# Kernel tuning notes

Measured on AMD Instinct MI355X. Metric: run time of the kernel, lower is better.

The kernel has to match this reference:

```python
import jax, jax.numpy as jnp
import numpy as np

B = 128          # graphs
N = 512          # nodes per graph
NT = B * N       # total nodes = 65536
E = NT * 16      # total edges = 1048576
IN = 64
H = 128
OUT = 2
L = 4            # num_layers
RATIO = 0.8


def setup_inputs() -> dict:
    key = jax.random.key(0)
    ks = jax.random.split(key, 20)

    def w(k, shape, fan_in):
        return jax.random.normal(k, shape, jnp.float32) / np.sqrt(fan_in)

    x = jax.random.normal(ks[0], (NT, IN), jnp.float32)
    edge_index = jax.random.randint(ks[1], (2, E), 0, NT, dtype=jnp.int32)
    batch = (jnp.arange(NT) // N).astype(jnp.int32)  # equal-size graphs

    return {
        "x": x,
        "edge_index": edge_index,
        "batch": batch,
        # conv1: GraphConv(IN, H, aggr='mean') -> lin_rel (w/ bias) + lin_root (no bias)
        "W1_rel": w(ks[2], (IN, H), IN),
        "W1_root": w(ks[3], (IN, H), IN),
        "b1": jnp.zeros((H,), jnp.float32),
        # convs[0..2]: GraphConv(H, H, aggr='mean'), stacked
        "Wc_rel": w(ks[4], (L - 1, H, H), H),
        "Wc_root": w(ks[5], (L - 1, H, H), H),
        "bc": jnp.zeros((L - 1, H), jnp.float32),
        # SAGPooling score GNN: GraphConv(H, 1) with default aggr='add'
        "pw_rel": w(ks[6], (H,), H),
        "pw_root": w(ks[7], (H,), H),
        "pb": jnp.zeros((1,), jnp.float32),
        # MLP head
        "lin1_W": w(ks[8], (L * H, H), L * H),
        "lin1_b": jnp.zeros((H,), jnp.float32),
        "lin2_W": w(ks[9], (H, OUT), H),
        "lin2_b": jnp.zeros((OUT,), jnp.float32),
    }


def _graph_conv_mean(x, src, dst, emask, W_rel, W_root, b, n):
    # PyG GraphConv: lin_rel(mean_{j->i} x_j) + lin_root(x_i); masked edges excluded.
    msg = x[src] * emask[:, None]                                  # [E, D] gather
    s = jax.ops.segment_sum(msg, dst, num_segments=n)              # [n, D] scatter-add
    cnt = jax.ops.segment_sum(emask, dst, num_segments=n)          # [n]
    agg = s / jnp.maximum(cnt, 1.0)[:, None]                       # zero for isolated nodes
    return agg @ W_rel + x @ W_root + b


def reference(x, edge_index, batch, W1_rel, W1_root, b1, Wc_rel, Wc_root, bc,
              pw_rel, pw_root, pb, lin1_W, lin1_b, lin2_W, lin2_b):
    src = edge_index[0]
    dst = edge_index[1]
    emask = jnp.ones((E,), jnp.float32)
    n = NT
    npg = N  # nodes per graph (all graphs equal size)

    h = jax.nn.relu(_graph_conv_mean(x, src, dst, emask, W1_rel, W1_root, b1, n))
    xs = [h.reshape(B, npg, H).mean(axis=1)]  # global_mean_pool

    for i in range(L - 1):
        h = jax.nn.relu(_graph_conv_mean(h, src, dst, emask, Wc_rel[i], Wc_root[i], bc[i], n))
        xs.append(h.reshape(B, npg, H).mean(axis=1))
        if i % 2 == 0 and i < L - 2:
            # ---- SAGPooling: score via GraphConv(H,1) with add aggregation ----
            smsg = jax.ops.segment_sum(h[src] * emask[:, None], dst, num_segments=n)
            score = smsg @ pw_rel + h @ pw_root + pb[0]            # [n]
            k = int(np.ceil(RATIO * npg))
            topv, topi = jax.lax.top_k(score.reshape(B, npg), k)   # per-graph top-k
            perm = (jnp.arange(B)[:, None] * npg + topi).reshape(-1)  # global kept ids
            h = h[perm] * jnp.tanh(topv.reshape(-1))[:, None]
            # remap edges; edges touching dropped nodes get masked out
            node_map = jnp.full((n,), -1, jnp.int32).at[perm].set(
                jnp.arange(B * k, dtype=jnp.int32))
            ns, nd = node_map[src], node_map[dst]
            keep = ((ns >= 0) & (nd >= 0)).astype(jnp.float32)
            emask = emask * keep
            src = jnp.where(ns >= 0, ns, 0)
            dst = jnp.where(nd >= 0, nd, 0)
            n = B * k
            npg = k

    xcat = jnp.concatenate(xs, axis=-1)                            # JumpingKnowledge 'cat'
    out = jax.nn.relu(xcat @ lin1_W + lin1_b)
    # dropout is identity in eval mode
    out = out @ lin2_W + lin2_b
    return jax.nn.log_softmax(out, axis=-1)
```

## Files before the change

kernel.cpp:

```cpp
#include <hip/hip_runtime.h>
#include <math.h>

#define NT 65536
#define EE 1048576
#define NB 128
#define KK 410
#define HH 128

typedef short bf16x8 __attribute__((ext_vector_type(8)));
typedef float f32x4 __attribute__((ext_vector_type(4)));

__device__ unsigned short g_xb[(size_t)NT * 64];
__device__ unsigned short g_hb1[(size_t)NT * HH];
__device__ unsigned short g_hb2[(size_t)NT * HH];
__device__ unsigned short g_wt1[128 * 128];
__device__ unsigned short g_wtc[3 * 128 * 256];
__device__ unsigned short g_csr1u[EE];
__device__ unsigned short g_keptu[NT];
__device__ unsigned int g_ebuck[EE];
__device__ int g_bcnt[128];
__device__ int g_bcur[128];
__device__ float g_trel[NT];
__device__ float g_troot[NT];
__device__ float g_gatef[NT];
__device__ float g_kinv[NT];
__device__ float g_xc16[4 * NB * 16 * 128];
__device__ int g_rows1[NT + 1];

__device__ __forceinline__ unsigned short* ubuf(int id) {
    switch (id) {
        case 0: return g_xb;
        case 1: return g_hb1;
        case 2: return g_hb2;
        case 3: return g_wt1;
        case 4: return g_wtc;
    }
    return g_xb;
}

__device__ __forceinline__ float b2f(unsigned short u) {
    union { unsigned int i; float f; } v;
    v.i = ((unsigned int)u) << 16;
    return v.f;
}
__device__ __forceinline__ unsigned short f2b(float f) {
    unsigned int x = __float_as_uint(f);
    unsigned int r = x + 0x7fffu + ((x >> 16) & 1u);
    return (unsigned short)(r >> 16);
}
__device__ __forceinline__ bf16x8 scale8(bf16x8 a, float g) {
    bf16x8 r;
#pragma unroll
    for (int i = 0; i < 8; i++) {
        unsigned short u = (unsigned short)a[i];
        r[i] = (short)f2b(b2f(u) * g);
    }
    return r;
}

__global__ __launch_bounds__(256) void k_prep(const float* __restrict__ x,
                                              const float* __restrict__ W1r,
                                              const float* __restrict__ W1o,
                                              const float* __restrict__ Wcr,
                                              const float* __restrict__ Wco,
                                              const int* __restrict__ dst) {
    if (blockIdx.x < 4544) {
        int tid = blockIdx.x * 256 + threadIdx.x;
        if (tid < 1048576) {
            float4 v = *(const float4*)&x[(size_t)tid * 4];
            unsigned int lo = (unsigned int)f2b(v.x) | ((unsigned int)f2b(v.y) << 16);
            unsigned int hi = (unsigned int)f2b(v.z) | ((unsigned int)f2b(v.w) << 16);
            *(uint2*)&g_xb[(size_t)tid * 4] = make_uint2(lo, hi);
        } else if (tid < 1048576 + 16384) {
            int r = tid - 1048576;
            int k = r & 127, n = r >> 7;
            float v = (k < 64) ? W1r[k * 128 + n] : W1o[(k - 64) * 128 + n];
            g_wt1[n * 128 + k] = f2b(v);
        } else {
            int r = tid - (1048576 + 16384);
            int l = r >> 15;
            int k = r & 255, n = (r >> 8) & 127;
            float v = (k < 128) ? Wcr[l * 16384 + k * 128 + n]
                                : Wco[l * 16384 + (k - 128) * 128 + n];
            g_wtc[l * 32768 + n * 256 + k] = f2b(v);
        }
    } else {
        __shared__ int h[128];
        if (threadIdx.x < 128) h[threadIdx.x] = 0;
        __syncthreads();
        int e0 = ((blockIdx.x - 4544) * 256 + threadIdx.x) * 4;
        int4 d = *(const int4*)&dst[e0];
        atomicAdd(&h[d.x >> 9], 1);
        atomicAdd(&h[d.y >> 9], 1);
        atomicAdd(&h[d.z >> 9], 1);
        atomicAdd(&h[d.w >> 9], 1);
        __syncthreads();
        if (threadIdx.x < 128 && h[threadIdx.x]) atomicAdd(&g_bcnt[threadIdx.x], h[threadIdx.x]);
    }
}

__global__ __launch_bounds__(256) void k_bscatter(const int* __restrict__ src,
                                                  const int* __restrict__ dst) {
    __shared__ int h[128];
    __shared__ int base[128];
    __shared__ int sc[128];
    __shared__ int vv[128];
    int t = threadIdx.x;
    if (t < 128) { vv[t] = g_bcnt[t]; sc[t] = vv[t]; h[t] = 0; }
    __syncthreads();
    for (int off = 1; off < 128; off <<= 1) {
        int u = (t >= off && t < 128) ? sc[t - off] : 0;
        __syncthreads();
        if (t < 128) sc[t] += u;
        __syncthreads();
    }
    int e0 = (blockIdx.x * 256 + t) * 4;
    int4 s = *(const int4*)&src[e0];
    int4 d = *(const int4*)&dst[e0];
    int b0 = d.x >> 9, b1 = d.y >> 9, b2 = d.z >> 9, b3 = d.w >> 9;
    atomicAdd(&h[b0], 1);
    atomicAdd(&h[b1], 1);
    atomicAdd(&h[b2], 1);
    atomicAdd(&h[b3], 1);
    __syncthreads();
    if (t < 128) {
        int c = h[t];
        base[t] = (sc[t] - vv[t]) + (c ? atomicAdd(&g_bcur[t], c) : 0);
        h[t] = 0;
    }
    __syncthreads();
    int r0 = atomicAdd(&h[b0], 1);
    g_ebuck[base[b0] + r0] = ((unsigned int)(d.x & 511) << 16) | (unsigned int)s.x;
    int r1 = atomicAdd(&h[b1], 1);
    g_ebuck[base[b1] + r1] = ((unsigned int)(d.y & 511) << 16) | (unsigned int)s.y;
    int r2 = atomicAdd(&h[b2], 1);
    g_ebuck[base[b2] + r2] = ((unsigned int)(d.z & 511) << 16) | (unsigned int)s.z;
    int r3 = atomicAdd(&h[b3], 1);
    g_ebuck[base[b3] + r3] = ((unsigned int)(d.w & 511) << 16) | (unsigned int)s.w;
}

__global__ __launch_bounds__(512) void k_bcsr() {
    __shared__ int hist[512];
    __shared__ int offs[512];
    __shared__ int cur[512];
    __shared__ int sc[128];
    int g = blockIdx.x, t = threadIdx.x;
    if (t < 128) sc[t] = g_bcnt[t];
    hist[t] = 0;
    cur[t] = 0;
    __syncthreads();
    for (int off = 1; off < 128; off <<= 1) {
        int u = (t >= off && t < 128) ? sc[t - off] : 0;
        __syncthreads();
        if (t < 128) sc[t] += u;
        __syncthreads();
    }
    int b0 = sc[g] - g_bcnt[g];
    int b1 = sc[g];
    for (int e = b0 + t; e < b1; e += 512) {
        unsigned int p = g_ebuck[e];
        atomicAdd(&hist[p >> 16], 1);
    }
    __syncthreads();
    int v = hist[t];
    offs[t] = v;
    __syncthreads();
    for (int off = 1; off < 512; off <<= 1) {
        int u = (t >= off) ? offs[t - off] : 0;
        __syncthreads();
        offs[t] += u;
        __syncthreads();
    }
    int excl = offs[t] - v;
    g_rows1[g * 512 + t] = b0 + excl;
    if (t == 511) g_rows1[g * 512 + 512] = b0 + excl + v;
    __syncthreads();
    offs[t] = excl;
    __syncthreads();
    for (int e = b0 + t; e < b1; e += 512) {
        unsigned int p = g_ebuck[e];
        int dl = p >> 16;
        int r = atomicAdd(&cur[dl], 1);
        g_csr1u[b0 + offs[dl] + r] = (unsigned short)(p & 0xFFFFu);
    }
}

template <int KA, int KB, int KC, int GATED, int MASKED, int DOTS, int BGATE>
__global__ __launch_bounds__(256, 8) void k_conv(int hId, int bId, int wId, int wOfs,
                                                 const float* __restrict__ bias, int outId,
                                                 int sec,
                                                 const float* __restrict__ pwr,
                                                 const float* __restrict__ pwt) {
    constexpr int NCHA = KA / 32;
    const int K = KA + KB;
    const unsigned short* h = ubuf(hId);
    const unsigned short* Bp = ubuf(bId);
    const unsigned short* Wt = ubuf(wId) + wOfs;
    unsigned short* out = ubuf(outId);
    __shared__ unsigned short part[2][16][136];
    __shared__ unsigned short frag[2][16][136];
    __shared__ float s[128];
    __shared__ float sdr[32], sdt[32];
    __shared__ int kcs[32];
    int lane = threadIdx.x & 63;
    int w = threadIdx.x >> 6;
    int g = w >> 1;
    int h2 = w & 1;
    int n16 = lane & 15, quad = lane >> 4;
    int rowbase = blockIdx.x * 32;
    int rowg = rowbase + g * 16;
    int node = rowg + n16;
    if (threadIdx.x < 128) s[threadIdx.x] = 0.f;
    if (threadIdx.x < 32) { sdr[threadIdx.x] = 0.f; sdt[threadIdx.x] = 0.f; }

    int r0 = g_rows1[node], r1 = g_rows1[node + 1];
    int mid = (r0 + r1) >> 1;
    int ea = h2 ? mid : r0;
    int eb = h2 ? r1 : mid;
    float aggacc[NCHA][8];
#pragma unroll
    for (int ch = 0; ch < NCHA; ch++)
#pragma unroll
        for (int j = 0; j < 8; j++) aggacc[ch][j] = 0.f;
    int kc = 0;
    const unsigned short* hq = h + quad * 8;
#define ACC8(arow, v, gf)                                        \
    arow[0] += gf * b2f((unsigned short)(v.x & 0xffff));         \
    arow[1] += gf * b2f((unsigned short)(v.x >> 16));            \
    arow[2] += gf * b2f((unsigned short)(v.y & 0xffff));         \
    arow[3] += gf * b2f((unsigned short)(v.y >> 16));            \
    arow[4] += gf * b2f((unsigned short)(v.z & 0xffff));         \
    arow[5] += gf * b2f((unsigned short)(v.z >> 16));            \
    arow[6] += gf * b2f((unsigned short)(v.w & 0xffff));         \
    arow[7] += gf * b2f((unsigned short)(v.w >> 16));
    int e = ea;
    for (; e + 2 <= eb; e += 2) {
        int i0 = g_csr1u[e], i1 = g_csr1u[e + 1];
        uint4 v0[NCHA], v1[NCHA];
#pragma unroll
        for (int ch = 0; ch < NCHA; ch++)
            v0[ch] = *(const uint4*)&hq[(size_t)i0 * KA + ch * 32];
#pragma unroll
        for (int ch = 0; ch < NCHA; ch++)
            v1[ch] = *(const uint4*)&hq[(size_t)i1 * KA + ch * 32];
        float gf0 = GATED ? g_gatef[i0] : 1.0f;
        float gf1 = GATED ? g_gatef[i1] : 1.0f;
        if (KC == 1) kc += (int)g_keptu[i0] + (int)g_keptu[i1];
#pragma unroll
        for (int ch = 0; ch < NCHA; ch++) { ACC8(aggacc[ch], v0[ch], gf0) }
#pragma unroll
        for (int ch = 0; ch < NCHA; ch++) { ACC8(aggacc[ch], v1[ch], gf1) }
    }
    if (e < eb) {
        int i0 = g_csr1u[e];
        uint4 v0[NCHA];
#pragma unroll
        for (int ch = 0; ch < NCHA; ch++)
            v0[ch] = *(const uint4*)&hq[(size_t)i0 * KA + ch * 32];
        float gf0 = GATED ? g_gatef[i0] : 1.0f;
        if (KC == 1) kc += (int)g_keptu[i0];
#pragma unroll
        for (int ch = 0; ch < NCHA; ch++) { ACC8(aggacc[ch], v0[ch], gf0) }
    }
#undef ACC8

    if (h2 == 0) {
#pragma unroll
        for (int ch = 0; ch < NCHA; ch++) {
            bf16x8 pk;
#pragma unroll
            for (int j = 0; j < 8; j++) pk[j] = (short)f2b(aggacc[ch][j]);
            *(bf16x8*)&part[g][n16][ch * 32 + quad * 8] = pk;
        }
        if (KC == 1 && quad == 0) kcs[g * 16 + n16] = kc;
    }
    __syncthreads();

    if (h2 == 1) {
#pragma unroll
        for (int ch = 0; ch < NCHA; ch++) {
            bf16x8 pv = *(const bf16x8*)&part[g][n16][ch * 32 + quad * 8];
#pragma unroll
            for (int j = 0; j < 8; j++) aggacc[ch][j] += b2f((unsigned short)pv[j]);
        }
        float inv;
        if (KC == 0) {
            int c = r1 - r0;
            inv = 1.0f / (float)(c > 0 ? c : 1);
        } else if (KC == 1) {
            kc += kcs[g * 16 + n16];
            inv = 1.0f / (float)(kc > 0 ? kc : 1);
            if (quad == 0) g_kinv[node] = inv;
        } else {
            inv = g_kinv[node];
        }
#pragma unroll
        for (int ch = 0; ch < NCHA; ch++) {
            bf16x8 fk;
#pragma unroll
            for (int j = 0; j < 8; j++) fk[j] = (short)f2b(aggacc[ch][j] * inv);
            *(bf16x8*)&frag[g][n16][ch * 32 + quad * 8] = fk;
        }
    }
    __syncthreads();

    float ga = BGATE ? g_gatef[node] : 1.0f;
    f32x4 acc[4];
#pragma unroll
    for (int c4 = 0; c4 < 4; c4++)
#pragma unroll
        for (int i = 0; i < 4; i++) acc[c4][i] = 0.f;
#pragma unroll
    for (int ks = 0; ks < K / 32; ks++) {
        bf16x8 a;
        if (ks < NCHA) {
            a = *(const bf16x8*)&frag[g][n16][ks * 32 + quad * 8];
        } else {
            int kk = (ks - NCHA) * 32;
            a = *(const bf16x8*)&Bp[(size_t)node * KB + kk + quad * 8];
            if (BGATE) a = scale8(a, ga);
        }
#pragma unroll
        for (int c4 = 0; c4 < 4; c4++) {
            int ct = h2 * 4 + c4;
            bf16x8 b = *(const bf16x8*)&Wt[(size_t)(ct * 16 + n16) * K + ks * 32 + quad * 8];
            acc[c4] = __builtin_amdgcn_mfma_f32_16x16x32_bf16(a, b, acc[c4], 0, 0, 0);
        }
    }

    {
        float m[4];
#pragma unroll
        for (int i = 0; i < 4; i++) {
            int r = rowg + quad * 4 + i;
            m[i] = (!MASKED || g_keptu[r]) ? 1.0f : 0.0f;
        }
#pragma unroll
        for (int c4 = 0; c4 < 4; c4++) {
            int c = (h2 * 4 + c4) * 16 + n16;
            float bv = bias[c];
#pragma unroll
            for (int i = 0; i < 4; i++) {
                int r = rowg + quad * 4 + i;
                float v = fmaxf(acc[c4][i] + bv, 0.f) * m[i];
                acc[c4][i] = v;
                out[(size_t)r * 128 + c] = f2b(v);
            }
        }
    }

#pragma unroll
    for (int c4 = 0; c4 < 4; c4++) {
        float p = acc[c4][0] + acc[c4][1] + acc[c4][2] + acc[c4][3];
        p += __shfl_xor(p, 16);
        p += __shfl_xor(p, 32);
        if (quad == 0) atomicAdd(&s[(h2 * 4 + c4) * 16 + n16], p);
    }

    if (DOTS) {
        float pr[4], pt[4];
#pragma unroll
        for (int c4 = 0; c4 < 4; c4++) {
            pr[c4] = pwr[(h2 * 4 + c4) * 16 + n16];
            pt[c4] = pwt[(h2 * 4 + c4) * 16 + n16];
        }
#pragma unroll
        for (int i = 0; i < 4; i++) {
            float dr = 0.f, dt = 0.f;
#pragma unroll
            for (int c4 = 0; c4 < 4; c4++) {
                dr += acc[c4][i] * pr[c4];
                dt += acc[c4][i] * pt[c4];
            }
            dr += __shfl_xor(dr, 1); dt += __shfl_xor(dt, 1);
            dr += __shfl_xor(dr, 2); dt += __shfl_xor(dt, 2);
            dr += __shfl_xor(dr, 4); dt += __shfl_xor(dt, 4);
            dr += __shfl_xor(dr, 8); dt += __shfl_xor(dt, 8);
            if (n16 == 0) {
                atomicAdd(&sdr[g * 16 + quad * 4 + i], dr);
                atomicAdd(&sdt[g * 16 + quad * 4 + i], dt);
            }
        }
    }
    __syncthreads();
    if (threadIdx.x < 128) {
        int gr = blockIdx.x >> 4, e16 = blockIdx.x & 15;
        g_xc16[((sec * NB + gr) * 16 + e16) * 128 + threadIdx.x] = s[threadIdx.x];
    }
    if (DOTS && threadIdx.x < 32) {
        g_trel[rowbase + threadIdx.x] = sdr[threadIdx.x];
        g_troot[rowbase + threadIdx.x] = sdt[threadIdx.x];
    }
}

__global__ __launch_bounds__(256) void k_topk(const float* __restrict__ pb) {
    __shared__ float sv[512];
    __shared__ int si[512];
    int g = blockIdx.x, t = threadIdx.x;
    if (t == 0) { g_bcnt[g] = 0; g_bcur[g] = 0; }
    float pbv = pb[0];
    for (int l = t; l < 512; l += 256) {
        int node = g * 512 + l;
        int r0 = g_rows1[node], r1 = g_rows1[node + 1];
        float s = 0.f;
        int e = r0;
        for (; e + 4 <= r1; e += 4) {
            float s0 = g_trel[g_csr1u[e]];
            float s1 = g_trel[g_csr1u[e + 1]];
            float s2 = g_trel[g_csr1u[e + 2]];
            float s3 = g_trel[g_csr1u[e + 3]];
            s += (s0 + s1) + (s2 + s3);
        }
        for (; e < r1; e++) s += g_trel[g_csr1u[e]];
        sv[l] = s + g_troot[node] + pbv;
        si[l] = l;
    }
    __syncthreads();
    for (int k = 2; k <= 512; k <<= 1) {
        for (int j = k >> 1; j > 0; j >>= 1) {
            for (int i = t; i < 512; i += 256) {
                int p = i ^ j;
                if (p > i) {
                    float va = sv[i], vb = sv[p];
                    int ia = si[i], ib = si[p];
                    bool aFirst = (va > vb) || (va == vb && ia < ib);
                    bool up = ((i & k) == 0);
                    if (up != aFirst) { sv[i] = vb; sv[p] = va; si[i] = ib; si[p] = ia; }
                }
            }
            __syncthreads();
        }
    }
    for (int r = t; r < 512; r += 256) {
        int old = g * 512 + si[r];
        if (r < KK) {
            g_gatef[old] = tanhf(sv[r]);
            g_keptu[old] = 1;
        } else {
            g_gatef[old] = 0.f;
            g_keptu[old] = 0;
        }
    }
}

__global__ __launch_bounds__(128) void k_head(const float* __restrict__ W1, const float* __restrict__ b1,
                                              const float* __restrict__ W2, const float* __restrict__ b2,
                                              float* __restrict__ out) {
    __shared__ float xr[512];
    __shared__ float r0[128], r1[128];
    int g = blockIdx.x, t = threadIdx.x;
    for (int i = t; i < 512; i += 128) {
        int sec = i >> 7, c = i & 127;
        const float* p = &g_xc16[((sec * NB + g) * 16) * 128 + c];
        float v = 0.f;
#pragma unroll
        for (int q = 0; q < 16; q++) v += p[q * 128];
        float inv = (sec < 2) ? (1.0f / 512.0f) : (1.0f / 410.0f);
        xr[i] = v * inv;
    }
    __syncthreads();
    float acc = b1[t];
    for (int k = 0; k < 512; k++) acc += xr[k] * W1[k * 128 + t];
    acc = fmaxf(acc, 0.f);
    r0[t] = acc * W2[t * 2 + 0];
    r1[t] = acc * W2[t * 2 + 1];
    __syncthreads();
    for (int off = 64; off > 0; off >>= 1) {
        if (t < off) { r0[t] += r0[t + off]; r1[t] += r1[t + off]; }
        __syncthreads();
    }
    if (t == 0) {
        float z0 = r0[0] + b2[0], z1 = r1[0] + b2[1];
        float m = fmaxf(z0, z1);
        float l = m + logf(expf(z0 - m) + expf(z1 - m));
        out[g * 2 + 0] = z0 - l;
        out[g * 2 + 1] = z1 - l;
    }
}

extern "C" void kernel_launch(void* const* d_in, const int* in_sizes, int n_in,
                              void* d_out, int out_size, void* d_ws, size_t ws_size,
                              hipStream_t stream) {
    const float* x = (const float*)d_in[0];
    const int* ei = (const int*)d_in[1];
    const int* src = ei;
    const int* dst = ei + EE;
    const float* W1r = (const float*)d_in[3];
    const float* W1o = (const float*)d_in[4];
    const float* b1 = (const float*)d_in[5];
    const float* Wcr = (const float*)d_in[6];
    const float* Wco = (const float*)d_in[7];
    const float* bc = (const float*)d_in[8];
    const float* pwr = (const float*)d_in[9];
    const float* pwt = (const float*)d_in[10];
    const float* pb = (const float*)d_in[11];
    const float* l1W = (const float*)d_in[12];
    const float* l1b = (const float*)d_in[13];
    const float* l2W = (const float*)d_in[14];
    const float* l2b = (const float*)d_in[15];
    float* out = (float*)d_out;

    k_prep<<<5568, 256, 0, stream>>>(x, W1r, W1o, Wcr, Wco, dst);

    k_bscatter<<<1024, 256, 0, stream>>>(src, dst);
    k_bcsr<<<128, 512, 0, stream>>>();

    k_conv<64, 64, 0, 0, 0, 0, 0><<<2048, 256, 0, stream>>>(0, 0, 3, 0, b1, 1, 0, pwr, pwt);

    k_conv<128, 128, 0, 0, 0, 1, 0><<<2048, 256, 0, stream>>>(1, 1, 4, 0, bc, 2, 1, pwr, pwt);

    k_topk<<<NB, 256, 0, stream>>>(pb);

    k_conv<128, 128, 1, 1, 1, 0, 1><<<2048, 256, 0, stream>>>(2, 2, 4, 32768, bc + 128, 1, 2, pwr, pwt);

    k_conv<128, 128, 2, 0, 1, 0, 0><<<2048, 256, 0, stream>>>(1, 1, 4, 65536, bc + 256, 2, 3, pwr, pwt);

    k_head<<<NB, 128, 0, stream>>>(l1W, l1b, l2W, l2b, out);
}
```

Before: 559.8 us.

## Split gather by feature halves across wave pairs and specialize first conv kernel

```diff
diff --git a/kernel.cpp b/kernel.cpp
--- a/kernel.cpp
+++ b/kernel.cpp
@@ -26,17 +26,6 @@
 __device__ float g_kinv[NT];
 __device__ float g_xc16[4 * NB * 16 * 128];
 __device__ int g_rows1[NT + 1];
-
-__device__ __forceinline__ unsigned short* ubuf(int id) {
-    switch (id) {
-        case 0: return g_xb;
-        case 1: return g_hb1;
-        case 2: return g_hb2;
-        case 3: return g_wt1;
-        case 4: return g_wtc;
-    }
-    return g_xb;
-}
 
 __device__ __forceinline__ float b2f(unsigned short u) {
     union { unsigned int i; float f; } v;
@@ -185,23 +174,115 @@
     }
 }
 
-template <int KA, int KB, int KC, int GATED, int MASKED, int DOTS, int BGATE>
-__global__ __launch_bounds__(256, 8) void k_conv(int hId, int bId, int wId, int wOfs,
-                                                 const float* __restrict__ bias, int outId,
+__global__ __launch_bounds__(256, 4) void k_conv1(const float* __restrict__ bias) {
+    const unsigned short* h = g_xb;
+    const unsigned short* Wt = g_wt1;
+    unsigned short* out = g_hb1;
+    __shared__ float s[128];
+    int lane = threadIdx.x & 63;
+    int w = threadIdx.x >> 6;
+    int n16 = lane & 15, quad = lane >> 4;
+    int rowbase = blockIdx.x * 64;
+    int rowg = rowbase + w * 16;
+    int node = rowg + n16;
+    if (threadIdx.x < 128) s[threadIdx.x] = 0.f;
+    int r0 = g_rows1[node], r1 = g_rows1[node + 1];
+    float aggacc[2][8];
+#pragma unroll
+    for (int ch = 0; ch < 2; ch++)
+#pragma unroll
+        for (int j = 0; j < 8; j++) aggacc[ch][j] = 0.f;
+    const unsigned short* hq = h + quad * 8;
+#define ACC8(arow, v)                                            \
+    arow[0] += b2f((unsigned short)(v.x & 0xffff));              \
+    arow[1] += b2f((unsigned short)(v.x >> 16));                 \
+    arow[2] += b2f((unsigned short)(v.y & 0xffff));              \
+    arow[3] += b2f((unsigned short)(v.y >> 16));                 \
+    arow[4] += b2f((unsigned short)(v.z & 0xffff));              \
+    arow[5] += b2f((unsigned short)(v.z >> 16));                 \
+    arow[6] += b2f((unsigned short)(v.w & 0xffff));              \
+    arow[7] += b2f((unsigned short)(v.w >> 16));
+    int e = r0;
+    for (; e + 2 <= r1; e += 2) {
+        int i0 = g_csr1u[e], i1 = g_csr1u[e + 1];
+        uint4 v00 = *(const uint4*)&hq[(size_t)i0 * 64];
+        uint4 v01 = *(const uint4*)&hq[(size_t)i0 * 64 + 32];
+        uint4 v10 = *(const uint4*)&hq[(size_t)i1 * 64];
+        uint4 v11 = *(const uint4*)&hq[(size_t)i1 * 64 + 32];
+        ACC8(aggacc[0], v00) ACC8(aggacc[1], v01)
+        ACC8(aggacc[0], v10) ACC8(aggacc[1], v11)
+    }
+    if (e < r1) {
+        int i0 = g_csr1u[e];
+        uint4 v00 = *(const uint4*)&hq[(size_t)i0 * 64];
+        uint4 v01 = *(const uint4*)&hq[(size_t)i0 * 64 + 32];
+        ACC8(aggacc[0], v00) ACC8(aggacc[1], v01)
+    }
+#undef ACC8
+    int c = r1 - r0;
+    float inv = 1.0f / (float)(c > 0 ? c : 1);
+    bf16x8 afrag[2];
+#pragma unroll
+    for (int ch = 0; ch < 2; ch++)
+#pragma unroll
+        for (int j = 0; j < 8; j++) afrag[ch][j] = (short)f2b(aggacc[ch][j] * inv);
+
+    f32x4 acc[8];
+#pragma unroll
+    for (int ct = 0; ct < 8; ct++)
+#pragma unroll
+        for (int i = 0; i < 4; i++) acc[ct][i] = 0.f;
+#pragma unroll
+    for (int ks = 0; ks < 4; ks++) {
+        bf16x8 a;
+        if (ks < 2) a = afrag[ks];
+        else a = *(const bf16x8*)&g_xb[(size_t)node * 64 + (ks - 2) * 32 + quad * 8];
+#pragma unroll
+        for (int ct = 0; ct < 8; ct++) {
+            bf16x8 b = *(const bf16x8*)&Wt[(size_t)(ct * 16 + n16) * 128 + ks * 32 + quad * 8];
+            acc[ct] = __builtin_amdgcn_mfma_f32_16x16x32_bf16(a, b, acc[ct], 0, 0, 0);
+        }
+    }
+#pragma unroll
+    for (int ct = 0; ct < 8; ct++) {
+        int cc = ct * 16 + n16;
+        float bv = bias[cc];
+#pragma unroll
+        for (int i = 0; i < 4; i++) {
+            int r = rowg + quad * 4 + i;
+            float v = fmaxf(acc[ct][i] + bv, 0.f);
+            acc[ct][i] = v;
+            out[(size_t)r * 128 + cc] = f2b(v);
+        }
+    }
+    __syncthreads();
+#pragma unroll
+    for (int ct = 0; ct < 8; ct++) {
+        float p = acc[ct][0] + acc[ct][1] + acc[ct][2] + acc[ct][3];
+        p += __shfl_xor(p, 16);
+        p += __shfl_xor(p, 32);
+        if (quad == 0) atomicAdd(&s[ct * 16 + n16], p);
+    }
+    __syncthreads();
+    if (threadIdx.x < 128) {
+        int gr = blockIdx.x >> 3, e8 = blockIdx.x & 7;
+        g_xc16[((0 * NB + gr) * 16 + e8) * 128 + threadIdx.x] = s[threadIdx.x];
+    }
+}
+
+template <int KC, int GATED, int MASKED, int DOTS, int BGATE>
+__global__ __launch_bounds__(256, 8) void k_conv(int hSel, int bSel, int wOfs,
+                                                 const float* __restrict__ bias, int outSel,
                                                  int sec,
                                                  const float* __restrict__ pwr,
                                                  const float* __restrict__ pwt) {
-    constexpr int NCHA = KA / 32;
-    const int K = KA + KB;
-    const unsigned short* h = ubuf(hId);
-    const unsigned short* Bp = ubuf(bId);
-    const unsigned short* Wt = ubuf(wId) + wOfs;
-    unsigned short* out = ubuf(outId);
-    __shared__ unsigned short part[2][16][136];
+    const unsigned short* h = hSel == 1 ? g_hb1 : g_hb2;
+    const unsigned short* Bp = bSel == 1 ? g_hb1 : g_hb2;
+    const unsigned short* Wt = g_wtc + wOfs;
+    unsigned short* out = outSel == 1 ? g_hb1 : g_hb2;
     __shared__ unsigned short frag[2][16][136];
     __shared__ float s[128];
     __shared__ float sdr[32], sdt[32];
-    __shared__ int kcs[32];
     int lane = threadIdx.x & 63;
     int w = threadIdx.x >> 6;
     int g = w >> 1;
@@ -214,16 +295,13 @@
     if (threadIdx.x < 32) { sdr[threadIdx.x] = 0.f; sdt[threadIdx.x] = 0.f; }
 
     int r0 = g_rows1[node], r1 = g_rows1[node + 1];
-    int mid = (r0 + r1) >> 1;
-    int ea = h2 ? mid : r0;
-    int eb = h2 ? r1 : mid;
-    float aggacc[NCHA][8];
-#pragma unroll
-    for (int ch = 0; ch < NCHA; ch++)
+    float aggacc[2][8];
+#pragma unroll
+    for (int ch = 0; ch < 2; ch++)
 #pragma unroll
         for (int j = 0; j < 8; j++) aggacc[ch][j] = 0.f;
     int kc = 0;
-    const unsigned short* hq = h + quad * 8;
+    const unsigned short* hq = h + h2 * 64 + quad * 8;
 #define ACC8(arow, v, gf)                                        \
     arow[0] += gf * b2f((unsigned short)(v.x & 0xffff));         \
     arow[1] += gf * b2f((unsigned short)(v.x >> 16));            \
@@ -233,74 +311,44 @@
     arow[5] += gf * b2f((unsigned short)(v.z >> 16));            \
     arow[6] += gf * b2f((unsigned short)(v.w & 0xffff));         \
     arow[7] += gf * b2f((unsigned short)(v.w >> 16));
-    int e = ea;
-    for (; e + 2 <= eb; e += 2) {
+    int e = r0;
+    for (; e + 2 <= r1; e += 2) {
         int i0 = g_csr1u[e], i1 = g_csr1u[e + 1];
-        uint4 v0[NCHA], v1[NCHA];
-#pragma unroll
-        for (int ch = 0; ch < NCHA; ch++)
-            v0[ch] = *(const uint4*)&hq[(size_t)i0 * KA + ch * 32];
-#pragma unroll
-        for (int ch = 0; ch < NCHA; ch++)
-            v1[ch] = *(const uint4*)&hq[(size_t)i1 * KA + ch * 32];
+        uint4 v00 = *(const uint4*)&hq[(size_t)i0 * 128];
+        uint4 v01 = *(const uint4*)&hq[(size_t)i0 * 128 + 32];
+        uint4 v10 = *(const uint4*)&hq[(size_t)i1 * 128];
+        uint4 v11 = *(const uint4*)&hq[(size_t)i1 * 128 + 32];
         float gf0 = GATED ? g_gatef[i0] : 1.0f;
         float gf1 = GATED ? g_gatef[i1] : 1.0f;
         if (KC == 1) kc += (int)g_keptu[i0] + (int)g_keptu[i1];
-#pragma unroll
-        for (int ch = 0; ch < NCHA; ch++) { ACC8(aggacc[ch], v0[ch], gf0) }
-#pragma unroll
-        for (int ch = 0; ch < NCHA; ch++) { ACC8(aggacc[ch], v1[ch], gf1) }
-    }
-    if (e < eb) {
+        ACC8(aggacc[0], v00, gf0) ACC8(aggacc[1], v01, gf0)
+        ACC8(aggacc[0], v10, gf1) ACC8(aggacc[1], v11, gf1)
+    }
+    if (e < r1) {
         int i0 = g_csr1u[e];
-        uint4 v0[NCHA];
-#pragma unroll
-        for (int ch = 0; ch < NCHA; ch++)
-            v0[ch] = *(const uint4*)&hq[(size_t)i0 * KA + ch * 32];
+        uint4 v00 = *(const uint4*)&hq[(size_t)i0 * 128];
+        uint4 v01 = *(const uint4*)&hq[(size_t)i0 * 128 + 32];
         float gf0 = GATED ? g_gatef[i0] : 1.0f;
         if (KC == 1) kc += (int)g_keptu[i0];
-#pragma unroll
-        for (int ch = 0; ch < NCHA; ch++) { ACC8(aggacc[ch], v0[ch], gf0) }
+        ACC8(aggacc[0], v00, gf0) ACC8(aggacc[1], v01, gf0)
     }
 #undef ACC8
-
-    if (h2 == 0) {
-#pragma unroll
-        for (int ch = 0; ch < NCHA; ch++) {
-            bf16x8 pk;
-#pragma unroll
-            for (int j = 0; j < 8; j++) pk[j] = (short)f2b(aggacc[ch][j]);
-            *(bf16x8*)&part[g][n16][ch * 32 + quad * 8] = pk;
-        }
-        if (KC == 1 && quad == 0) kcs[g * 16 + n16] = kc;
-    }
-    __syncthreads();
-
-    if (h2 == 1) {
-#pragma unroll
-        for (int ch = 0; ch < NCHA; ch++) {
-            bf16x8 pv = *(const bf16x8*)&part[g][n16][ch * 32 + quad * 8];
-#pragma unroll
-            for (int j = 0; j < 8; j++) aggacc[ch][j] += b2f((unsigned short)pv[j]);
-        }
-        float inv;
-        if (KC == 0) {
-            int c = r1 - r0;
-            inv = 1.0f / (float)(c > 0 ? c : 1);
-        } else if (KC == 1) {
-            kc += kcs[g * 16 + n16];
-            inv = 1.0f / (float)(kc > 0 ? kc : 1);
-            if (quad == 0) g_kinv[node] = inv;
-        } else {
-            inv = g_kinv[node];
-        }
-#pragma unroll
-        for (int ch = 0; ch < NCHA; ch++) {
-            bf16x8 fk;
-#pragma unroll
-            for (int j = 0; j < 8; j++) fk[j] = (short)f2b(aggacc[ch][j] * inv);
-            *(bf16x8*)&frag[g][n16][ch * 32 + quad * 8] = fk;
-        }
+    float inv;
+    if (KC == 0) {
+        int c = r1 - r0;
+        inv = 1.0f / (float)(c > 0 ? c : 1);
+    } else if (KC == 1) {
+        inv = 1.0f / (float)(kc > 0 ? kc : 1);
+        if (h2 == 0 && quad == 0) g_kinv[node] = inv;
+    } else {
+        inv = g_kinv[node];
+    }
+#pragma unroll
+    for (int ch = 0; ch < 2; ch++) {
+        bf16x8 fk;
+#pragma unroll
+        for (int j = 0; j < 8; j++) fk[j] = (short)f2b(aggacc[ch][j] * inv);
+        *(bf16x8*)&frag[g][n16][h2 * 64 + ch * 32 + quad * 8] = fk;
     }
     __syncthreads();
 
@@ -311,19 +359,18 @@
 #pragma unroll
         for (int i = 0; i < 4; i++) acc[c4][i] = 0.f;
 #pragma unroll
-    for (int ks = 0; ks < K / 32; ks++) {
+    for (int ks = 0; ks < 8; ks++) {
         bf16x8 a;
-        if (ks < NCHA) {
+        if (ks < 4) {
             a = *(const bf16x8*)&frag[g][n16][ks * 32 + quad * 8];
         } else {
-            int kk = (ks - NCHA) * 32;
-            a = *(const bf16x8*)&Bp[(size_t)node * KB + kk + quad * 8];
+            a = *(const bf16x8*)&Bp[(size_t)node * 128 + (ks - 4) * 32 + quad * 8];
             if (BGATE) a = scale8(a, ga);
         }
 #pragma unroll
         for (int c4 = 0; c4 < 4; c4++) {
             int ct = h2 * 4 + c4;
-            bf16x8 b = *(const bf16x8*)&Wt[(size_t)(ct * 16 + n16) * K + ks * 32 + quad * 8];
+            bf16x8 b = *(const bf16x8*)&Wt[(size_t)(ct * 16 + n16) * 256 + ks * 32 + quad * 8];
             acc[c4] = __builtin_amdgcn_mfma_f32_16x16x32_bf16(a, b, acc[c4], 0, 0, 0);
         }
     }
@@ -452,9 +499,9 @@
     for (int i = t; i < 512; i += 128) {
         int sec = i >> 7, c = i & 127;
         const float* p = &g_xc16[((sec * NB + g) * 16) * 128 + c];
+        int nq = (sec == 0) ? 8 : 16;
         float v = 0.f;
-#pragma unroll
-        for (int q = 0; q < 16; q++) v += p[q * 128];
+        for (int q = 0; q < nq; q++) v += p[q * 128];
         float inv = (sec < 2) ? (1.0f / 512.0f) : (1.0f / 410.0f);
         xr[i] = v * inv;
     }
@@ -505,15 +552,15 @@
     k_bscatter<<<1024, 256, 0, stream>>>(src, dst);
     k_bcsr<<<128, 512, 0, stream>>>();
 
-    k_conv<64, 64, 0, 0, 0, 0, 0><<<2048, 256, 0, stream>>>(0, 0, 3, 0, b1, 1, 0, pwr, pwt);
-
-    k_conv<128, 128, 0, 0, 0, 1, 0><<<2048, 256, 0, stream>>>(1, 1, 4, 0, bc, 2, 1, pwr, pwt);
+    k_conv1<<<1024, 256, 0, stream>>>(b1);
+
+    k_conv<0, 0, 0, 1, 0><<<2048, 256, 0, stream>>>(1, 1, 0, bc, 2, 1, pwr, pwt);
 
     k_topk<<<NB, 256, 0, stream>>>(pb);
 
-    k_conv<128, 128, 1, 1, 1, 0, 1><<<2048, 256, 0, stream>>>(2, 2, 4, 32768, bc + 128, 1, 2, pwr, pwt);
-
-    k_conv<128, 128, 2, 0, 1, 0, 0><<<2048, 256, 0, stream>>>(1, 1, 4, 65536, bc + 256, 2, 3, pwr, pwt);
+    k_conv<1, 1, 1, 0, 1><<<2048, 256, 0, stream>>>(2, 2, 32768, bc + 128, 1, 2, pwr, pwt);
+
+    k_conv<2, 0, 1, 0, 0><<<2048, 256, 0, stream>>>(1, 1, 65536, bc + 256, 2, 3, pwr, pwt);
 
     k_head<<<NB, 128, 0, stream>>>(l1W, l1b, l2W, l2b, out);
 }
```

Result: faster. 527.2 us (-5.8%).
